# Kernel tuning notes

Hardware: AMD Instinct MI355X
Metric: run time of the kernel (lower is better)

The kernel has to match this reference:

```python
import jax, jax.numpy as jnp
import numpy as np

N = 86016      # 1024 graphs x 84 nodes
E = 4194304    # directed edges
H = 32         # hidden size
B = 1024       # graphs per batch
NPG = 84       # nodes per graph (hardcoded in original forward)
DEPTH = 4      # args.depth
NEG_SLOPE = 0.2


def setup_inputs() -> dict:
    key = jax.random.key(0)
    ks = jax.random.split(key, 12)
    s = 0.1
    return {
        "x": jax.random.normal(ks[0], (N, 1), jnp.float32),
        "edge_index": jax.random.randint(ks[1], (2, E), 0, N, jnp.int64 if jax.config.jax_enable_x64 else jnp.int32),
        "edge_attr": jax.random.normal(ks[2], (E, 2), jnp.float32),
        "W0": jax.random.normal(ks[3], (1, H), jnp.float32) * s,
        "Ws": jax.random.normal(ks[4], (DEPTH - 1, H, H), jnp.float32) * s,
        "att_src": jax.random.normal(ks[5], (DEPTH, H), jnp.float32) * s,
        "att_dst": jax.random.normal(ks[6], (DEPTH, H), jnp.float32) * s,
        "We": jax.random.normal(ks[7], (DEPTH, 2, H), jnp.float32) * s,
        "att_edge": jax.random.normal(ks[8], (DEPTH, H), jnp.float32) * s,
        "bias": jnp.zeros((DEPTH, H), jnp.float32),
        "lin_w": jax.random.normal(ks[9], (H, 1), jnp.float32) * s,
        "lin_b": jnp.zeros((1,), jnp.float32),
    }


def _gat_layer(h_in, src, dst, ea, W, a_s, a_d, We_l, a_e, b):
    """PyG GATConv, heads=1, edge_dim set, self-loops already appended.
    src/dst: [E+N] indices; ea: [E+N, edge_dim] edge attrs (with mean-filled loops)."""
    h = h_in @ W                                  # [N, H]
    alpha_src = h @ a_s                           # [N]
    alpha_dst = h @ a_d                           # [N]
    # fold lin_edge + att_edge: (ea @ We) @ a_e == ea @ (We @ a_e) -> avoids [E,H]
    alpha_edge = ea @ (We_l @ a_e)                # [E+N]
    logits = alpha_src[src] + alpha_dst[dst] + alpha_edge
    logits = jnp.where(logits >= 0, logits, NEG_SLOPE * logits)  # leaky_relu(0.2)
    # segment softmax over destination nodes (every node has a self-loop -> nonempty)
    m = jax.ops.segment_max(logits, dst, num_segments=N)
    w = jnp.exp(logits - m[dst])
    denom = jax.ops.segment_sum(w, dst, num_segments=N)
    alpha = w / denom[dst]                        # [E+N]
    out = jax.ops.segment_sum(alpha[:, None] * h[src], dst, num_segments=N)
    return out + b


def reference(x, edge_index, edge_attr, W0, Ws, att_src, att_dst, We, att_edge, bias, lin_w, lin_b):
    src0, dst0 = edge_index[0], edge_index[1]
    # add_self_loops with fill_value='mean': per-dst mean of incoming edge attrs
    deg = jax.ops.segment_sum(jnp.ones((E,), x.dtype), dst0, num_segments=N)
    ea_loop = jax.ops.segment_sum(edge_attr, dst0, num_segments=N) / jnp.maximum(deg, 1.0)[:, None]
    loops = jnp.arange(N, dtype=src0.dtype)
    src = jnp.concatenate([src0, loops])
    dst = jnp.concatenate([dst0, loops])
    ea = jnp.concatenate([edge_attr, ea_loop], axis=0)

    # layer 0 (+ relu; dropout is identity in eval)
    h = _gat_layer(x, src, dst, ea, W0, att_src[0], att_dst[0], We[0], att_edge[0], bias[0])
    h = jax.nn.relu(h)
    # middle layers
    for i in range(1, DEPTH - 1):
        h = _gat_layer(h, src, dst, ea, Ws[i - 1], att_src[i], att_dst[i], We[i], att_edge[i], bias[i])
        h = jax.nn.relu(h)
    # last layer: no relu/dropout
    h = _gat_layer(h, src, dst, ea, Ws[DEPTH - 2], att_src[DEPTH - 1], att_dst[DEPTH - 1],
                   We[DEPTH - 1], att_edge[DEPTH - 1], bias[DEPTH - 1])

    # global_add_pool over 84-node graphs, then linear + relu
    graph_ids = jnp.repeat(jnp.arange(B), NPG)    # [N]
    pooled = jax.ops.segment_sum(h, graph_ids, num_segments=B)  # [B, H]
    return jax.nn.relu(pooled @ lin_w + lin_b)    # [B, 1]
```

## Files before the change

kernel.cpp:

```cpp
#include <hip/hip_runtime.h>

#define N_NODES 86016
#define N_EDGES 4194304
#define HID 32
#define B_GR 1024
#define NPG 84
#define NEG 0.2f

#define NCH 512
#define CHE 8192
#define NB  512
#define NPB 168
#define SRCMASK 0x1FFFF

typedef float floatx2 __attribute__((ext_vector_type(2)));

constexpr size_t O_REC   = 0;
constexpr size_t O_CM    = O_REC  + (size_t)N_EDGES * 8;
constexpr size_t O_HT    = O_CM   + (size_t)NB * NCH * 4;
constexpr size_t O_HB    = O_HT   + (size_t)N_NODES * HID;
constexpr size_t O_AS    = O_HB   + (size_t)N_NODES * HID * 4;
constexpr size_t O_AD    = O_AS   + (size_t)N_NODES * 4;
constexpr size_t O_ROW   = O_AD   + (size_t)N_NODES * 4;
constexpr size_t O_BTOT  = O_ROW  + (size_t)(N_NODES + 1) * 4 + 12;
constexpr size_t O_BBASE = O_BTOT + (size_t)NB * 4;
constexpr size_t O_FOLD  = O_BBASE + (size_t)(NB + 1) * 4 + 12;

__device__ __forceinline__ unsigned short f2bf(float f) {
    unsigned u = __float_as_uint(f);
    u += 0x7FFFu + ((u >> 16) & 1u);
    return (unsigned short)(u >> 16);
}

__global__ __launch_bounds__(1024) void k_hist(const int* __restrict__ dst, int* __restrict__ cm) {
    __shared__ int cnt[NB];
    int t = threadIdx.x, c = blockIdx.x;
    if (t < NB) cnt[t] = 0;
    __syncthreads();
    int base = c * CHE;
#pragma unroll
    for (int k = 0; k < 8; ++k) {
        int d = dst[base + k * 1024 + t];
        atomicAdd(&cnt[(unsigned)d / NPB], 1);
    }
    __syncthreads();
    if (t < NB) cm[t * NCH + c] = cnt[t];
}

__global__ __launch_bounds__(512) void k_scanchunks(int* __restrict__ cm, int* __restrict__ btot) {
    __shared__ int sa[NCH], sb[NCH];
    int b = blockIdx.x, t = threadIdx.x;
    sa[t] = cm[b * NCH + t];
    __syncthreads();
    int* s = sa; int* d = sb;
    for (int off = 1; off < NCH; off <<= 1) {
        d[t] = s[t] + (t >= off ? s[t - off] : 0);
        __syncthreads();
        int* tmp = s; s = d; d = tmp;
    }
    cm[b * NCH + t] = t ? s[t - 1] : 0;
    if (t == 0) btot[b] = s[NCH - 1];
}

__global__ void k_scanbuckets(const int* __restrict__ btot, int* __restrict__ bbase,
                              int* __restrict__ row,
                              const float* __restrict__ We, const float* __restrict__ ae,
                              float* __restrict__ fold) {
    __shared__ int sa[NB], sb[NB];
    int t = threadIdx.x;
    if (t < 8) {
        int l = t >> 1, c = t & 1;
        float s = 0.f;
        for (int j = 0; j < 32; ++j) s += We[l * 64 + c * 32 + j] * ae[l * 32 + j];
        fold[t] = s;
    }
    sa[t] = btot[t];
    __syncthreads();
    int* s = sa; int* d = sb;
    for (int off = 1; off < NB; off <<= 1) {
        d[t] = s[t] + (t >= off ? s[t - off] : 0);
        __syncthreads();
        int* tmp = s; s = d; d = tmp;
    }
    bbase[t] = t ? s[t - 1] : 0;
    if (t == NB - 1) { bbase[NB] = s[NB - 1]; row[N_NODES] = s[NB - 1]; }
}

__global__ __launch_bounds__(1024) void k_place(const int* __restrict__ ei,
                                                const float2* __restrict__ ea,
                                                const int* __restrict__ cm,
                                                const int* __restrict__ bbase,
                                                int2* __restrict__ rec) {
    __shared__ int cnt[NB];
    __shared__ int base[NB];
    int t = threadIdx.x, c = blockIdx.x;
    if (t < NB) cnt[t] = 0;
    __syncthreads();
    int eb = c * CHE;
    int wd0[8], bin[8], rnk[8];
    unsigned pk[8];
#pragma unroll
    for (int k = 0; k < 8; ++k) {
        int e = eb + k * 1024 + t;
        int s = ei[e];
        int d = ei[N_EDGES + e];
        float2 a = ea[e];
        int b = (unsigned)d / NPB;
        int dn = d - b * NPB;
        wd0[k] = s | (dn << 17);
        pk[k] = ((unsigned)f2bf(a.y) << 16) | f2bf(a.x);
        bin[k] = b;
        rnk[k] = atomicAdd(&cnt[b], 1);
    }
    __syncthreads();
    if (t < NB) base[t] = bbase[t] + cm[t * NCH + c];
    __syncthreads();
#pragma unroll
    for (int k = 0; k < 8; ++k)
        rec[base[bin[k]] + rnk[k]] = make_int2(wd0[k], (int)pk[k]);
}

__global__ __launch_bounds__(1024) void k_sort(int2* __restrict__ rec,
                                               const int* __restrict__ bbase,
                                               int* __restrict__ row) {
    __shared__ int cnt[256], tmp[256], ebase[256];
    int b = blockIdx.x, t = threadIdx.x;
    int n0 = b * NPB;
    int beg = bbase[b], end = bbase[b + 1], m = end - beg;
    if (t < 256) cnt[t] = 0;
    __syncthreads();
    int2 rv[12];
    int dr[12];
    int cv = 0;
    for (int i = t; i < m; i += 1024) {
        int2 r = rec[beg + i];
        int dn = ((unsigned)r.x >> 17) & 0xFF;
        int rnk = atomicAdd(&cnt[dn], 1);
        if (cv < 12) { rv[cv] = r; dr[cv] = dn | (rnk << 8); }
        cv++;
    }
    __syncthreads();
    int* s = cnt; int* d = tmp;
    for (int off = 1; off < 256; off <<= 1) {
        int v = 0;
        if (t < 256) v = s[t] + (t >= off ? s[t - off] : 0);
        __syncthreads();
        if (t < 256) d[t] = v;
        __syncthreads();
        int* tp = s; s = d; d = tp;
    }
    if (t < 256) ebase[t] = t ? s[t - 1] : 0;
    __syncthreads();
    if (t < NPB) row[n0 + t] = beg + ebase[t];
    int ncv = cv < 12 ? cv : 12;
    for (int k = 0; k < ncv; ++k) {
        int dn = dr[k] & 0xFF;
        int rnk = dr[k] >> 8;
        rec[beg + ebase[dn] + rnk] = rv[k];
    }
}

__device__ __forceinline__ void store_fp8_pair(unsigned short* __restrict__ hout,
                                               int n, int j, float acc) {
    float p = __shfl_xor(acc, 1);
    if (!(j & 1)) {
        int pk = __builtin_amdgcn_cvt_pk_fp8_f32(acc, p, 0, false);
        hout[(n << 4) + (j >> 1)] = (unsigned short)pk;
    }
}

__global__ void k_transform0(const float* __restrict__ x, const float* __restrict__ W0,
                             const float* __restrict__ as_w, const float* __restrict__ ad_w,
                             unsigned short* __restrict__ hout, float* __restrict__ as_arr,
                             float* __restrict__ ad_arr) {
    int tid = blockIdx.x * 256 + threadIdx.x;
    int j = tid & 31;
    int n = tid >> 5;
    float acc = x[n] * W0[j];
    store_fp8_pair(hout, n, j, acc);
    float v1 = acc * as_w[j], v2 = acc * ad_w[j];
#pragma unroll
    for (int m = 16; m >= 1; m >>= 1) {
        v1 += __shfl_xor(v1, m);
        v2 += __shfl_xor(v2, m);
    }
    if (j == 0) { as_arr[n] = v1; ad_arr[n] = v2; }
}

__global__ void k_transform(const float* __restrict__ hin, const float* __restrict__ W,
                            const float* __restrict__ as_w, const float* __restrict__ ad_w,
                            unsigned short* __restrict__ hout, float* __restrict__ as_arr,
                            float* __restrict__ ad_arr) {
    __shared__ float Wl[1024];
    int t = threadIdx.x;
#pragma unroll
    for (int i = 0; i < 4; ++i) Wl[t + i * 256] = W[t + i * 256];
    __syncthreads();
    int tid = blockIdx.x * 256 + t;
    int j = tid & 31;
    int n = tid >> 5;
    float hv = hin[tid];
    float acc = 0.f;
#pragma unroll
    for (int k = 0; k < 32; ++k) acc += __shfl(hv, k, 32) * Wl[k * 32 + j];
    store_fp8_pair(hout, n, j, acc);
    float v1 = acc * as_w[j], v2 = acc * ad_w[j];
#pragma unroll
    for (int m = 16; m >= 1; m >>= 1) {
        v1 += __shfl_xor(v1, m);
        v2 += __shfl_xor(v2, m);
    }
    if (j == 0) { as_arr[n] = v1; ad_arr[n] = v2; }
}

__device__ __forceinline__ void acc_word(float wp, int word, floatx2* acc) {
    floatx2 v01 = __builtin_amdgcn_cvt_pk_f32_fp8(word, false);
    floatx2 v23 = __builtin_amdgcn_cvt_pk_f32_fp8(word, true);
    floatx2 w2 = {wp, wp};
    acc[0] = __builtin_elementwise_fma(w2, v01, acc[0]);
    acc[1] = __builtin_elementwise_fma(w2, v23, acc[1]);
}

__global__ void k_gather(const unsigned short* __restrict__ hT, const int2* __restrict__ rec,
                         const int* __restrict__ row,
                         const float* __restrict__ as_arr, const float* __restrict__ ad_arr,
                         const float* __restrict__ fold, const float* __restrict__ bias,
                         float* __restrict__ out, int do_relu) {
    const int* hw = (const int*)hT;
    __shared__ int2 exch[4][2][64];
    int lane = threadIdx.x & 63;
    int wv = threadIdx.x >> 6;
    int slot = lane >> 3;
    int dl = lane & 7;
    int n0 = blockIdx.x * 8 + wv * 2;
    int n1 = n0 + 1;
    int beg0 = row[n0], end0 = row[n0 + 1];
    int beg1 = row[n1], end1 = row[n1 + 1];
    float cd0 = ad_arr[n0], cd1 = ad_arr[n1];
    float f0 = fold[0], f1 = fold[1];
    floatx2 zz = {0.f, 0.f};
    floatx2 accA[2] = {zz, zz};
    floatx2 accB[2] = {zz, zz};
    float den0 = 0.f, esum0 = 0.f, den1 = 0.f, esum1 = 0.f;
    for (int e0 = beg0, e1 = beg1; (e0 < end0) || (e1 < end1); e0 += 64, e1 += 64) {
        int ee0 = e0 + lane, ee1 = e1 + lane;
        int i0 = ee0 < end0 ? ee0 : end0 - 1; i0 = i0 < 0 ? 0 : i0;
        int i1 = ee1 < end1 ? ee1 : end1 - 1; i1 = i1 < 0 ? 0 : i1;
        int2 r0 = rec[i0];
        int2 r1 = rec[i1];
        int s0 = r0.x & SRCMASK;
        int s1 = r1.x & SRCMASK;
        float a0 = as_arr[s0];
        float a1 = as_arr[s1];
        float ax0 = __uint_as_float((unsigned)r0.y << 16);
        float ay0 = __uint_as_float((unsigned)r0.y & 0xFFFF0000u);
        float ax1 = __uint_as_float((unsigned)r1.y << 16);
        float ay1 = __uint_as_float((unsigned)r1.y & 0xFFFF0000u);
        float ed0 = fmaf(ax0, f0, ay0 * f1);
        float ed1 = fmaf(ax1, f0, ay1 * f1);
        float lg0 = a0 + cd0 + ed0;
        float lg1 = a1 + cd1 + ed1;
        lg0 = fmaxf(lg0, NEG * lg0);
        lg1 = fmaxf(lg1, NEG * lg1);
        bool act0 = ee0 < end0, act1 = ee1 < end1;
        float w0 = act0 ? __expf(lg0) : 0.f;
        float w1 = act1 ? __expf(lg1) : 0.f;
        den0 += w0; den1 += w1;
        esum0 += act0 ? ed0 : 0.f;
        esum1 += act1 ? ed1 : 0.f;
        exch[wv][0][lane] = make_int2(s0, __float_as_int(w0));
        exch[wv][1][lane] = make_int2(s1, __float_as_int(w1));
#pragma unroll
        for (int p = 0; p < 8; ++p) {
            int sl = p * 8 + slot;
            int2 sw0 = exch[wv][0][sl];
            int2 sw1 = exch[wv][1][sl];
            int h0 = hw[(sw0.x << 3) + dl];
            int h1 = hw[(sw1.x << 3) + dl];
            acc_word(__int_as_float(sw0.y), h0, accA);
            acc_word(__int_as_float(sw1.y), h1, accB);
        }
    }
    float* fA = (float*)accA;
    float* fB = (float*)accB;
#pragma unroll
    for (int m = 8; m <= 32; m <<= 1) {
#pragma unroll
        for (int k = 0; k < 4; ++k) {
            fA[k] += __shfl_xor(fA[k], m);
            fB[k] += __shfl_xor(fB[k], m);
        }
    }
#pragma unroll
    for (int m = 1; m <= 32; m <<= 1) {
        den0 += __shfl_xor(den0, m);
        den1 += __shfl_xor(den1, m);
        esum0 += __shfl_xor(esum0, m);
        esum1 += __shfl_xor(esum1, m);
    }
    int dg0 = end0 - beg0, dg1 = end1 - beg1;
    float el0 = esum0 / fmaxf((float)dg0, 1.0f);
    float el1 = esum1 / fmaxf((float)dg1, 1.0f);
    float lgs0 = as_arr[n0] + cd0 + el0;
    float lgs1 = as_arr[n1] + cd1 + el1;
    lgs0 = fmaxf(lgs0, NEG * lgs0);
    lgs1 = fmaxf(lgs1, NEG * lgs1);
    float ws0 = __expf(lgs0), ws1 = __expf(lgs1);
    den0 += ws0; den1 += ws1;
    int hs0 = hw[(n0 << 3) + dl];
    int hs1 = hw[(n1 << 3) + dl];
    acc_word(ws0, hs0, accA);
    acc_word(ws1, hs1, accB);
    float rd0 = 1.0f / den0, rd1 = 1.0f / den1;
    float4 bi = *(const float4*)(bias + 4 * dl);
    float4 o0 = {fA[0] * rd0 + bi.x, fA[1] * rd0 + bi.y, fA[2] * rd0 + bi.z, fA[3] * rd0 + bi.w};
    float4 o1 = {fB[0] * rd1 + bi.x, fB[1] * rd1 + bi.y, fB[2] * rd1 + bi.z, fB[3] * rd1 + bi.w};
    if (do_relu) {
        o0.x = fmaxf(o0.x, 0.f); o0.y = fmaxf(o0.y, 0.f);
        o0.z = fmaxf(o0.z, 0.f); o0.w = fmaxf(o0.w, 0.f);
        o1.x = fmaxf(o1.x, 0.f); o1.y = fmaxf(o1.y, 0.f);
        o1.z = fmaxf(o1.z, 0.f); o1.w = fmaxf(o1.w, 0.f);
    }
    if (slot == 0) {
        *(float4*)(out + (n0 << 5) + (dl << 2)) = o0;
        *(float4*)(out + (n1 << 5) + (dl << 2)) = o1;
    }
}

__global__ void k_pool(const float* __restrict__ h, const float* __restrict__ lw,
                       const float* __restrict__ lb, float* __restrict__ out) {
    int lane = threadIdx.x & 63;
    int g = blockIdx.x * 4 + (threadIdx.x >> 6);
    int j = lane & 31;
    int half = lane >> 5;
    const float* base = h + (size_t)g * NPG * HID;
    float acc = 0.f;
    for (int i = half; i < NPG; i += 2) acc += base[i * HID + j];
    acc += __shfl_xor(acc, 32);
    float v = acc * lw[j];
#pragma unroll
    for (int m = 16; m >= 1; m >>= 1) v += __shfl_xor(v, m);
    if (lane == 0) out[g] = fmaxf(v + lb[0], 0.f);
}

extern "C" void kernel_launch(void* const* d_in, const int* in_sizes, int n_in,
                              void* d_out, int out_size, void* d_ws, size_t ws_size,
                              hipStream_t stream) {
    const float* x        = (const float*)d_in[0];
    const int*   ei       = (const int*)d_in[1];
    const float* eattr    = (const float*)d_in[2];
    const float* W0       = (const float*)d_in[3];
    const float* Ws       = (const float*)d_in[4];
    const float* att_src  = (const float*)d_in[5];
    const float* att_dst  = (const float*)d_in[6];
    const float* We       = (const float*)d_in[7];
    const float* att_edge = (const float*)d_in[8];
    const float* bias     = (const float*)d_in[9];
    const float* lin_w    = (const float*)d_in[10];
    const float* lin_b    = (const float*)d_in[11];
    float* out = (float*)d_out;

    char* w = (char*)d_ws;
    int2*           rec    = (int2*)(w + O_REC);
    int*            cm     = (int*)(w + O_CM);
    unsigned short* hT     = (unsigned short*)(w + O_HT);
    float*          hB     = (float*)(w + O_HB);
    float*          as_arr = (float*)(w + O_AS);
    float*          ad_arr = (float*)(w + O_AD);
    int*            row    = (int*)(w + O_ROW);
    int*            btot   = (int*)(w + O_BTOT);
    int*            bbase  = (int*)(w + O_BBASE);
    float*          fold   = (float*)(w + O_FOLD);

    k_hist<<<NCH, 1024, 0, stream>>>(ei + N_EDGES, cm);
    k_scanchunks<<<NB, 512, 0, stream>>>(cm, btot);
    k_scanbuckets<<<1, NB, 0, stream>>>(btot, bbase, row, We, att_edge, fold);
    k_place<<<NCH, 1024, 0, stream>>>(ei, (const float2*)eattr, cm, bbase, rec);
    k_sort<<<NB, 1024, 0, stream>>>(rec, bbase, row);

    k_transform0<<<N_NODES * HID / 256, 256, 0, stream>>>(x, W0, att_src, att_dst,
                                                          hT, as_arr, ad_arr);
    k_gather<<<N_NODES / 8, 256, 0, stream>>>(hT, rec, row, as_arr, ad_arr,
                                              fold, bias, hB, 1);
    for (int l = 1; l < 4; ++l) {
        k_transform<<<N_NODES * HID / 256, 256, 0, stream>>>(
            hB, Ws + (size_t)(l - 1) * HID * HID, att_src + l * HID, att_dst + l * HID,
            hT, as_arr, ad_arr);
        k_gather<<<N_NODES / 8, 256, 0, stream>>>(hT, rec, row, as_arr, ad_arr,
                                                  fold + 2 * l, bias + l * HID, hB,
                                                  (l < 3) ? 1 : 0);
    }

    k_pool<<<B_GR / 4, 256, 0, stream>>>(hB, lin_w, lin_b, out);
}
```

Before: 481.1 us.

## Process eight nodes per wave in gather with prefetched edge records

Each wave in the gather kernel now handles eight destination nodes in four pairs instead of one pair, and the grid shrinks accordingly. The first 64 edge records for all four pairs are loaded up front, and each pair issues its feature-row gathers before the softmax math. A rare loop covers nodes with more than 64 edges. The aim is more memory-level parallelism to hide random-gather latency, at the cost of higher register pressure and fewer waves in the grid.

```diff
diff --git a/kernel.cpp b/kernel.cpp
--- a/kernel.cpp
+++ b/kernel.cpp
@@ -227,103 +227,160 @@
                          const float* __restrict__ fold, const float* __restrict__ bias,
                          float* __restrict__ out, int do_relu) {
     const int* hw = (const int*)hT;
-    __shared__ int2 exch[4][2][64];
+    __shared__ int   exS[4][2][64];
+    __shared__ float exW[4][2][64];
     int lane = threadIdx.x & 63;
     int wv = threadIdx.x >> 6;
     int slot = lane >> 3;
     int dl = lane & 7;
-    int n0 = blockIdx.x * 8 + wv * 2;
-    int n1 = n0 + 1;
-    int beg0 = row[n0], end0 = row[n0 + 1];
-    int beg1 = row[n1], end1 = row[n1 + 1];
-    float cd0 = ad_arr[n0], cd1 = ad_arr[n1];
+    const int* hwd = hw + dl;
+    int nb = blockIdx.x * 32 + wv * 8;
+    int rowv[9];
+#pragma unroll
+    for (int i = 0; i < 9; ++i) rowv[i] = row[nb + i];
     float f0 = fold[0], f1 = fold[1];
+    float4 bi = *(const float4*)(bias + 4 * dl);
     floatx2 zz = {0.f, 0.f};
-    floatx2 accA[2] = {zz, zz};
-    floatx2 accB[2] = {zz, zz};
-    float den0 = 0.f, esum0 = 0.f, den1 = 0.f, esum1 = 0.f;
-    for (int e0 = beg0, e1 = beg1; (e0 < end0) || (e1 < end1); e0 += 64, e1 += 64) {
-        int ee0 = e0 + lane, ee1 = e1 + lane;
-        int i0 = ee0 < end0 ? ee0 : end0 - 1; i0 = i0 < 0 ? 0 : i0;
-        int i1 = ee1 < end1 ? ee1 : end1 - 1; i1 = i1 < 0 ? 0 : i1;
-        int2 r0 = rec[i0];
-        int2 r1 = rec[i1];
-        int s0 = r0.x & SRCMASK;
-        int s1 = r1.x & SRCMASK;
-        float a0 = as_arr[s0];
-        float a1 = as_arr[s1];
-        float ax0 = __uint_as_float((unsigned)r0.y << 16);
-        float ay0 = __uint_as_float((unsigned)r0.y & 0xFFFF0000u);
-        float ax1 = __uint_as_float((unsigned)r1.y << 16);
-        float ay1 = __uint_as_float((unsigned)r1.y & 0xFFFF0000u);
+
+    int2 r0[4], r1[4];
+#pragma unroll
+    for (int k = 0; k < 4; ++k) {
+        int beg0 = rowv[2 * k], end0 = rowv[2 * k + 1];
+        int beg1 = rowv[2 * k + 1], end1 = rowv[2 * k + 2];
+        int i0 = beg0 + lane; i0 = (i0 < end0) ? i0 : 0;
+        int i1 = beg1 + lane; i1 = (i1 < end1) ? i1 : 0;
+        r0[k] = rec[i0];
+        r1[k] = rec[i1];
+    }
+
+#pragma unroll
+    for (int k = 0; k < 4; ++k) {
+        int beg0 = rowv[2 * k], end0 = rowv[2 * k + 1];
+        int beg1 = rowv[2 * k + 1], end1 = rowv[2 * k + 2];
+        int n0 = nb + 2 * k, n1 = n0 + 1;
+        bool act0 = (beg0 + lane) < end0;
+        bool act1 = (beg1 + lane) < end1;
+        int s0 = r0[k].x & SRCMASK;
+        int s1 = r1[k].x & SRCMASK;
+        exS[wv][0][lane] = s0 << 3;
+        exS[wv][1][lane] = s1 << 3;
+        int h0[8], h1[8];
+#pragma unroll
+        for (int p = 0; p < 8; ++p) {
+            int sp0 = exS[wv][0][p * 8 + slot];
+            int sp1 = exS[wv][1][p * 8 + slot];
+            h0[p] = hwd[sp0];
+            h1[p] = hwd[sp1];
+        }
+        float a0 = as_arr[s0], a1 = as_arr[s1];
+        float cd0 = ad_arr[n0], cd1 = ad_arr[n1];
+        float ax0 = __uint_as_float((unsigned)r0[k].y << 16);
+        float ay0 = __uint_as_float((unsigned)r0[k].y & 0xFFFF0000u);
+        float ax1 = __uint_as_float((unsigned)r1[k].y << 16);
+        float ay1 = __uint_as_float((unsigned)r1[k].y & 0xFFFF0000u);
         float ed0 = fmaf(ax0, f0, ay0 * f1);
         float ed1 = fmaf(ax1, f0, ay1 * f1);
-        float lg0 = a0 + cd0 + ed0;
-        float lg1 = a1 + cd1 + ed1;
-        lg0 = fmaxf(lg0, NEG * lg0);
-        lg1 = fmaxf(lg1, NEG * lg1);
-        bool act0 = ee0 < end0, act1 = ee1 < end1;
+        float lg0 = a0 + cd0 + ed0; lg0 = fmaxf(lg0, NEG * lg0);
+        float lg1 = a1 + cd1 + ed1; lg1 = fmaxf(lg1, NEG * lg1);
         float w0 = act0 ? __expf(lg0) : 0.f;
         float w1 = act1 ? __expf(lg1) : 0.f;
-        den0 += w0; den1 += w1;
-        esum0 += act0 ? ed0 : 0.f;
-        esum1 += act1 ? ed1 : 0.f;
-        exch[wv][0][lane] = make_int2(s0, __float_as_int(w0));
-        exch[wv][1][lane] = make_int2(s1, __float_as_int(w1));
+        exW[wv][0][lane] = w0;
+        exW[wv][1][lane] = w1;
+        float den0 = w0, den1 = w1;
+        float es0 = act0 ? ed0 : 0.f;
+        float es1 = act1 ? ed1 : 0.f;
+        floatx2 acc0[2] = {zz, zz};
+        floatx2 acc1[2] = {zz, zz};
 #pragma unroll
         for (int p = 0; p < 8; ++p) {
-            int sl = p * 8 + slot;
-            int2 sw0 = exch[wv][0][sl];
-            int2 sw1 = exch[wv][1][sl];
-            int h0 = hw[(sw0.x << 3) + dl];
-            int h1 = hw[(sw1.x << 3) + dl];
-            acc_word(__int_as_float(sw0.y), h0, accA);
-            acc_word(__int_as_float(sw1.y), h1, accB);
-        }
-    }
-    float* fA = (float*)accA;
-    float* fB = (float*)accB;
-#pragma unroll
-    for (int m = 8; m <= 32; m <<= 1) {
-#pragma unroll
-        for (int k = 0; k < 4; ++k) {
-            fA[k] += __shfl_xor(fA[k], m);
-            fB[k] += __shfl_xor(fB[k], m);
-        }
-    }
-#pragma unroll
-    for (int m = 1; m <= 32; m <<= 1) {
-        den0 += __shfl_xor(den0, m);
-        den1 += __shfl_xor(den1, m);
-        esum0 += __shfl_xor(esum0, m);
-        esum1 += __shfl_xor(esum1, m);
-    }
-    int dg0 = end0 - beg0, dg1 = end1 - beg1;
-    float el0 = esum0 / fmaxf((float)dg0, 1.0f);
-    float el1 = esum1 / fmaxf((float)dg1, 1.0f);
-    float lgs0 = as_arr[n0] + cd0 + el0;
-    float lgs1 = as_arr[n1] + cd1 + el1;
-    lgs0 = fmaxf(lgs0, NEG * lgs0);
-    lgs1 = fmaxf(lgs1, NEG * lgs1);
-    float ws0 = __expf(lgs0), ws1 = __expf(lgs1);
-    den0 += ws0; den1 += ws1;
-    int hs0 = hw[(n0 << 3) + dl];
-    int hs1 = hw[(n1 << 3) + dl];
-    acc_word(ws0, hs0, accA);
-    acc_word(ws1, hs1, accB);
-    float rd0 = 1.0f / den0, rd1 = 1.0f / den1;
-    float4 bi = *(const float4*)(bias + 4 * dl);
-    float4 o0 = {fA[0] * rd0 + bi.x, fA[1] * rd0 + bi.y, fA[2] * rd0 + bi.z, fA[3] * rd0 + bi.w};
-    float4 o1 = {fB[0] * rd1 + bi.x, fB[1] * rd1 + bi.y, fB[2] * rd1 + bi.z, fB[3] * rd1 + bi.w};
-    if (do_relu) {
-        o0.x = fmaxf(o0.x, 0.f); o0.y = fmaxf(o0.y, 0.f);
-        o0.z = fmaxf(o0.z, 0.f); o0.w = fmaxf(o0.w, 0.f);
-        o1.x = fmaxf(o1.x, 0.f); o1.y = fmaxf(o1.y, 0.f);
-        o1.z = fmaxf(o1.z, 0.f); o1.w = fmaxf(o1.w, 0.f);
-    }
-    if (slot == 0) {
-        *(float4*)(out + (n0 << 5) + (dl << 2)) = o0;
-        *(float4*)(out + (n1 << 5) + (dl << 2)) = o1;
+            float wp0 = exW[wv][0][p * 8 + slot];
+            float wp1 = exW[wv][1][p * 8 + slot];
+            acc_word(wp0, h0[p], acc0);
+            acc_word(wp1, h1[p], acc1);
+        }
+        if (end0 - beg0 > 64 || end1 - beg1 > 64) {
+            for (int e0 = beg0 + 64, e1 = beg1 + 64; e0 < end0 || e1 < end1;
+                 e0 += 64, e1 += 64) {
+                int i0 = e0 + lane; bool c0 = i0 < end0; i0 = c0 ? i0 : 0;
+                int i1 = e1 + lane; bool c1 = i1 < end1; i1 = c1 ? i1 : 0;
+                int2 q0 = rec[i0], q1 = rec[i1];
+                int t0 = q0.x & SRCMASK, t1 = q1.x & SRCMASK;
+                exS[wv][0][lane] = t0 << 3;
+                exS[wv][1][lane] = t1 << 3;
+                int g0[8], g1[8];
+#pragma unroll
+                for (int p = 0; p < 8; ++p) {
+                    int sp0 = exS[wv][0][p * 8 + slot];
+                    int sp1 = exS[wv][1][p * 8 + slot];
+                    g0[p] = hwd[sp0];
+                    g1[p] = hwd[sp1];
+                }
+                float b0 = as_arr[t0], b1 = as_arr[t1];
+                float bx0 = __uint_as_float((unsigned)q0.y << 16);
+                float by0 = __uint_as_float((unsigned)q0.y & 0xFFFF0000u);
+                float bx1 = __uint_as_float((unsigned)q1.y << 16);
+                float by1 = __uint_as_float((unsigned)q1.y & 0xFFFF0000u);
+                float fd0 = fmaf(bx0, f0, by0 * f1);
+                float fd1 = fmaf(bx1, f0, by1 * f1);
+                float mg0 = b0 + cd0 + fd0; mg0 = fmaxf(mg0, NEG * mg0);
+                float mg1 = b1 + cd1 + fd1; mg1 = fmaxf(mg1, NEG * mg1);
+                float v0 = c0 ? __expf(mg0) : 0.f;
+                float v1 = c1 ? __expf(mg1) : 0.f;
+                exW[wv][0][lane] = v0;
+                exW[wv][1][lane] = v1;
+                den0 += v0; den1 += v1;
+                es0 += c0 ? fd0 : 0.f;
+                es1 += c1 ? fd1 : 0.f;
+#pragma unroll
+                for (int p = 0; p < 8; ++p) {
+                    float wp0 = exW[wv][0][p * 8 + slot];
+                    float wp1 = exW[wv][1][p * 8 + slot];
+                    acc_word(wp0, g0[p], acc0);
+                    acc_word(wp1, g1[p], acc1);
+                }
+            }
+        }
+        float* fA = (float*)acc0;
+        float* fB = (float*)acc1;
+#pragma unroll
+        for (int m = 8; m <= 32; m <<= 1) {
+#pragma unroll
+            for (int q = 0; q < 4; ++q) {
+                fA[q] += __shfl_xor(fA[q], m);
+                fB[q] += __shfl_xor(fB[q], m);
+            }
+        }
+#pragma unroll
+        for (int m = 1; m <= 32; m <<= 1) {
+            den0 += __shfl_xor(den0, m);
+            den1 += __shfl_xor(den1, m);
+            es0 += __shfl_xor(es0, m);
+            es1 += __shfl_xor(es1, m);
+        }
+        int dg0 = end0 - beg0, dg1 = end1 - beg1;
+        float el0 = es0 / fmaxf((float)dg0, 1.0f);
+        float el1 = es1 / fmaxf((float)dg1, 1.0f);
+        float lgs0 = as_arr[n0] + cd0 + el0; lgs0 = fmaxf(lgs0, NEG * lgs0);
+        float lgs1 = as_arr[n1] + cd1 + el1; lgs1 = fmaxf(lgs1, NEG * lgs1);
+        float ws0 = __expf(lgs0), ws1 = __expf(lgs1);
+        den0 += ws0; den1 += ws1;
+        acc_word(ws0, hwd[n0 << 3], acc0);
+        acc_word(ws1, hwd[n1 << 3], acc1);
+        float rd0 = 1.0f / den0, rd1 = 1.0f / den1;
+        float4 o0 = {fA[0] * rd0 + bi.x, fA[1] * rd0 + bi.y,
+                     fA[2] * rd0 + bi.z, fA[3] * rd0 + bi.w};
+        float4 o1 = {fB[0] * rd1 + bi.x, fB[1] * rd1 + bi.y,
+                     fB[2] * rd1 + bi.z, fB[3] * rd1 + bi.w};
+        if (do_relu) {
+            o0.x = fmaxf(o0.x, 0.f); o0.y = fmaxf(o0.y, 0.f);
+            o0.z = fmaxf(o0.z, 0.f); o0.w = fmaxf(o0.w, 0.f);
+            o1.x = fmaxf(o1.x, 0.f); o1.y = fmaxf(o1.y, 0.f);
+            o1.z = fmaxf(o1.z, 0.f); o1.w = fmaxf(o1.w, 0.f);
+        }
+        if (slot == 0) {
+            *(float4*)(out + (n0 << 5) + (dl << 2)) = o0;
+            *(float4*)(out + (n1 << 5) + (dl << 2)) = o1;
+        }
     }
 }
 
@@ -380,15 +437,15 @@
 
     k_transform0<<<N_NODES * HID / 256, 256, 0, stream>>>(x, W0, att_src, att_dst,
                                                           hT, as_arr, ad_arr);
-    k_gather<<<N_NODES / 8, 256, 0, stream>>>(hT, rec, row, as_arr, ad_arr,
-                                              fold, bias, hB, 1);
+    k_gather<<<N_NODES / 32, 256, 0, stream>>>(hT, rec, row, as_arr, ad_arr,
+                                               fold, bias, hB, 1);
     for (int l = 1; l < 4; ++l) {
         k_transform<<<N_NODES * HID / 256, 256, 0, stream>>>(
             hB, Ws + (size_t)(l - 1) * HID * HID, att_src + l * HID, att_dst + l * HID,
             hT, as_arr, ad_arr);
-        k_gather<<<N_NODES / 8, 256, 0, stream>>>(hT, rec, row, as_arr, ad_arr,
-                                                  fold + 2 * l, bias + l * HID, hB,
-                                                  (l < 3) ? 1 : 0);
+        k_gather<<<N_NODES / 32, 256, 0, stream>>>(hT, rec, row, as_arr, ad_arr,
+                                                   fold + 2 * l, bias + l * HID, hB,
+                                                   (l < 3) ? 1 : 0);
     }
 
     k_pool<<<B_GR / 4, 256, 0, stream>>>(hB, lin_w, lin_b, out);
```

Measured after the change: 485.8 us. Within noise of the previous version (+1.0%).
